# Kernel tuning notes

Measured on AMD Instinct MI355X. Metric: run time of the kernel, lower is better.

The kernel has to match this reference:

```python
import jax, jax.numpy as jnp
import numpy as np

N_COMP = 8
N_BASIS = 16
N_FEATURES = 64
N_CAT = 8
N_CONT = 56
N_UNIQUE = 100
BATCH = 32768
T0, T1 = 0.0, 10.0
SEP = 1e-3  # constants.MIN_TRANSITION_POINT_SEP
SIGNS = np.array([1.0, -1.0, 1.0, -1.0, 1.0, -1.0, 1.0, -1.0], dtype=np.float32)
CONT_IDX = np.arange(N_CONT)
CAT_IDX = np.arange(N_CONT, N_FEATURES)


def _offset():
    # torch_inverse_softplus(avg_interval_per_feature)
    v = (T1 - T0) / N_COMP / (N_FEATURES + 1)
    return float(np.log(np.exp(v) - 1.0))


def setup_inputs():
    key = jax.random.key(0)
    ks = jax.random.split(key, 11)
    off = _offset()
    B = jax.random.normal(ks[0], (BATCH, N_CONT, N_BASIS), jnp.float32)
    codes = jax.random.randint(ks[1], (BATCH, N_CAT), 0, N_UNIQUE)
    B_cat = jax.nn.one_hot(codes, N_UNIQUE, dtype=jnp.float32).reshape(BATCH, N_CAT * N_UNIQUE)
    Wh = jax.random.normal(ks[2], (N_BASIS, N_CONT, N_COMP), jnp.float32) + off
    Wh_cat = jax.random.normal(ks[3], (N_CAT, N_UNIQUE, N_COMP), jnp.float32) + off
    bh = jax.random.normal(ks[4], (N_COMP,), jnp.float32) + off
    Wv = jax.random.normal(ks[5], (N_BASIS, N_CONT, N_COMP), jnp.float32)
    Wv_cat = jax.random.normal(ks[6], (N_CAT, N_UNIQUE, N_COMP), jnp.float32)
    bv = jax.random.normal(ks[7], (N_COMP,), jnp.float32)
    Wic = jax.random.normal(ks[8], (N_BASIS, N_CONT, 1), jnp.float32)
    Wic_cat = jax.random.normal(ks[9], (N_CAT, N_UNIQUE, 1), jnp.float32)
    bic = jax.random.normal(ks[10], (1,), jnp.float32)
    return {"B": B, "B_cat": B_cat, "Wh": Wh, "Wh_cat": Wh_cat, "bh": bh,
            "Wv": Wv, "Wv_cat": Wv_cat, "bv": bv,
            "Wic": Wic, "Wic_cat": Wic_cat, "bic": bic}


def _calculate_gams(B, B_cat, W, W_cat, bias, positive):
    # continuous: per-feature small matmul  (b,i,k) x (k,i,c) -> (b,c,i)
    cont = jnp.einsum('bik,kic->bci', B, W)
    # categorical: one-hot gather expressed as blockwise matmul  (b,f,n) x (f,n,c) -> (b,c,f)
    cat = jnp.einsum('bfn,fnc->bcf', B_cat.reshape(B.shape[0], N_CAT, N_UNIQUE), W_cat)
    c = W.shape[2]
    out = jnp.zeros((B.shape[0], c, N_FEATURES + 1), dtype=B.dtype)
    out = out.at[:, :, CONT_IDX].set(cont)
    out = out.at[:, :, CAT_IDX].set(cat)
    out = out.at[:, :, -1].set(bias[None, :])
    return jax.nn.softplus(out) if positive else out


def reference(B, B_cat, Wh, Wh_cat, bh, Wv, Wv_cat, bv, Wic, Wic_cat, bic):
    H = _calculate_gams(B, B_cat, Wh, Wh_cat, bh, True)      # (b, n_comp, n_feat+1)
    V = _calculate_gams(B, B_cat, Wv, Wv_cat, bv, True)      # (b, n_comp, n_feat+1)
    IC = _calculate_gams(B, B_cat, Wic, Wic_cat, bic, False)  # (b, 1, n_feat+1)
    b = B.shape[0]
    signs = jnp.asarray(SIGNS)
    h_sum = H.sum(-1)   # (b, n_comp) per-segment horizontal increments
    v_sum = V.sum(-1)
    sep = SEP * jnp.arange(1, N_COMP + 1, dtype=B.dtype)
    # sequential cumulative build == prefix sums over the composition axis
    t = jnp.concatenate([jnp.full((b, 1), T0, B.dtype),
                         T0 + jnp.cumsum(h_sum, axis=1) + sep], axis=1)  # (b, n_comp+1)
    x0 = IC.sum(-1)     # (b, 1)
    x = jnp.concatenate([x0, x0 + jnp.cumsum(signs * v_sum, axis=1)], axis=1)
    # bounded composition: clamp the last horizontal coordinate
    t = t.at[:, -1].set(jnp.maximum(t[:, -2] + SEP, T1))
    return jnp.stack([t, x], axis=-1)  # (b, n_comp+1, 2)
```

## Files before the change

### kernel.cpp

```cpp
#include <hip/hip_runtime.h>

#define NCOMP 8
#define NCONT 56
#define NCAT 8
#define NU 100
#define NROWS 32768
#define SEPC 1e-3f
#define T1F 10.0f

#define WST 132
#define WICST 20

__device__ __forceinline__ float sp(float x) {
    return fmaxf(x, 0.0f) + __logf(1.0f + __expf(-fabsf(x)));
}

__device__ __forceinline__ float dot4(float4 a, float4 b) {
    return fmaf(a.x, b.x, fmaf(a.y, b.y, fmaf(a.z, b.z, a.w * b.w)));
}

__global__ __launch_bounds__(1024) void tpm_kernel(
    const float* __restrict__ B, const float* __restrict__ Bcat,
    const float* __restrict__ Wh, const float* __restrict__ Whc, const float* __restrict__ bh,
    const float* __restrict__ Wv, const float* __restrict__ Wvc, const float* __restrict__ bv,
    const float* __restrict__ Wic, const float* __restrict__ Wicc, const float* __restrict__ bic,
    float* __restrict__ out)
{
    __shared__ float sWh[NCONT * WST];
    __shared__ float sWv[NCONT * WST];
    __shared__ float sWic[NCONT * WICST];
    __shared__ int   sCode[16][NCAT];

    const int tid = threadIdx.x;

    for (int idx = tid; idx < NCONT * 128; idx += 1024) {
        int i = idx >> 7, rem = idx & 127;
        int c = rem >> 4, k = rem & 15;
        sWh[i * WST + rem] = Wh[(k * NCONT + i) * NCOMP + c];
        sWv[i * WST + rem] = Wv[(k * NCONT + i) * NCOMP + c];
    }
    for (int idx = tid; idx < NCONT * 16; idx += 1024) {
        int i = idx >> 4, k = idx & 15;
        sWic[i * WICST + k] = Wic[k * NCONT + i];
    }
    __syncthreads();

    const int lane = tid & 63;
    const int widx = tid >> 6;
    const int gw = (blockIdx.x << 4) + widx;
    const int nw = gridDim.x << 4;

    float bhs[NCOMP], bvs[NCOMP];
#pragma unroll
    for (int c = 0; c < NCOMP; ++c) { bhs[c] = sp(bh[c]); bvs[c] = sp(bv[c]); }
    const float bic0 = bic[0];

    for (int r = gw; r < NROWS; r += nw) {
        const float4* pc = (const float4*)(Bcat + (size_t)r * 800);
#pragma unroll
        for (int it = 0; it < 4; ++it) {
            int v = it * 64 + lane;
            if (v < 200) {
                float4 q = pc[v];
                int n = v * 4;
                if (q.x > 0.5f) sCode[widx][(n + 0) / NU] = (n + 0) % NU;
                if (q.y > 0.5f) sCode[widx][(n + 1) / NU] = (n + 1) % NU;
                if (q.z > 0.5f) sCode[widx][(n + 2) / NU] = (n + 2) % NU;
                if (q.w > 0.5f) sCode[widx][(n + 3) / NU] = (n + 3) % NU;
            }
        }
        __threadfence_block();

        float h[NCOMP], w[NCOMP], ic;
        if (lane < NCONT) {
            const float4* pB = (const float4*)(B + (size_t)r * 896 + lane * 16);
            float4 b0 = pB[0], b1 = pB[1], b2 = pB[2], b3 = pB[3];
            const float4* ph = (const float4*)(&sWh[lane * WST]);
            const float4* pv = (const float4*)(&sWv[lane * WST]);
#pragma unroll
            for (int c = 0; c < NCOMP; ++c) {
                h[c] = dot4(b0, ph[c * 4 + 0]) + dot4(b1, ph[c * 4 + 1]) +
                       dot4(b2, ph[c * 4 + 2]) + dot4(b3, ph[c * 4 + 3]);
                w[c] = dot4(b0, pv[c * 4 + 0]) + dot4(b1, pv[c * 4 + 1]) +
                       dot4(b2, pv[c * 4 + 2]) + dot4(b3, pv[c * 4 + 3]);
            }
            const float4* pi = (const float4*)(&sWic[lane * WICST]);
            ic = dot4(b0, pi[0]) + dot4(b1, pi[1]) + dot4(b2, pi[2]) + dot4(b3, pi[3]);
        } else {
            int f = lane - NCONT;
            int g = f * NU + sCode[widx][f];
            const float4* qh = (const float4*)(Whc + g * 8);
            const float4* qv = (const float4*)(Wvc + g * 8);
            float4 a0 = qh[0], a1 = qh[1];
            float4 c0 = qv[0], c1 = qv[1];
            h[0] = a0.x; h[1] = a0.y; h[2] = a0.z; h[3] = a0.w;
            h[4] = a1.x; h[5] = a1.y; h[6] = a1.z; h[7] = a1.w;
            w[0] = c0.x; w[1] = c0.y; w[2] = c0.z; w[3] = c0.w;
            w[4] = c1.x; w[5] = c1.y; w[6] = c1.z; w[7] = c1.w;
            ic = Wicc[g];
        }

#pragma unroll
        for (int c = 0; c < NCOMP; ++c) { h[c] = sp(h[c]); w[c] = sp(w[c]); }

#pragma unroll
        for (int off = 32; off >= 1; off >>= 1) {
#pragma unroll
            for (int c = 0; c < NCOMP; ++c) {
                h[c] += __shfl_xor(h[c], off, 64);
                w[c] += __shfl_xor(w[c], off, 64);
            }
            ic += __shfl_xor(ic, off, 64);
        }
#pragma unroll
        for (int c = 0; c < NCOMP; ++c) { h[c] += bhs[c]; w[c] += bvs[c]; }
        ic += bic0;

        if (lane < 9) {
            int m = (lane == 8) ? 7 : lane;
            float tj = SEPC * (float)lane;
            float xj = ic;
#pragma unroll
            for (int c = 0; c < NCOMP; ++c) {
                if (c < m)    tj += h[c];
                if (c < lane) xj += (c & 1) ? -w[c] : w[c];
            }
            if (lane == 8) tj = fmaxf(tj, T1F);
            float2 o; o.x = tj; o.y = xj;
            ((float2*)(out + (size_t)r * 18))[lane] = o;
        }
    }
}

extern "C" void kernel_launch(void* const* d_in, const int* in_sizes, int n_in,
                              void* d_out, int out_size, void* d_ws, size_t ws_size,
                              hipStream_t stream) {
    (void)in_sizes; (void)n_in; (void)out_size; (void)d_ws; (void)ws_size;
    const float* B    = (const float*)d_in[0];
    const float* Bcat = (const float*)d_in[1];
    const float* Wh   = (const float*)d_in[2];
    const float* Whc  = (const float*)d_in[3];
    const float* bh   = (const float*)d_in[4];
    const float* Wv   = (const float*)d_in[5];
    const float* Wvc  = (const float*)d_in[6];
    const float* bv   = (const float*)d_in[7];
    const float* Wic  = (const float*)d_in[8];
    const float* Wicc = (const float*)d_in[9];
    const float* bic  = (const float*)d_in[10];
    float* out = (float*)d_out;

    hipLaunchKernelGGL(tpm_kernel, dim3(256), dim3(1024), 0, stream,
                       B, Bcat, Wh, Whc, bh, Wv, Wvc, bv, Wic, Wicc, bic, out);
}
```

Measured before the change: 282.9 us.

## Use packed fp16 dot products, fp16 shuffle reductions, and branchless code decode

Converts the continuous weights and B rows to packed fp16 and computes the per-feature dot products with v_dot2 instructions. The H/V softplus outputs are packed into half2 pairs so the cross-lane reduction needs half as many shuffles. It also decodes each one-hot float4 arithmetically into a single store, moves the bias softplus into shared memory, simplifies softplus to an exp2/log form, and doubles the grid to 512 blocks with a launch-bounds hint. These changes cut ALU work, shuffles and register use, at the cost of fp16 precision in the matmul and in the sums of up to 64 softplus values, which may break tolerance. The new softplus can also overflow for large inputs.

```diff
diff --git a/kernel.cpp b/kernel.cpp
--- a/kernel.cpp
+++ b/kernel.cpp
@@ -8,41 +8,73 @@
 #define SEPC 1e-3f
 #define T1F 10.0f
 
-#define WST 132
-#define WICST 20
+typedef __fp16 f16x2 __attribute__((ext_vector_type(2)));
+typedef _Float16 h2arith __attribute__((ext_vector_type(2)));
+
+#define HSTRIDE 17
+#define ICSTRIDE 3
+
+union H8 { f16x2 h2[4]; float4 f4; };
 
 __device__ __forceinline__ float sp(float x) {
-    return fmaxf(x, 0.0f) + __logf(1.0f + __expf(-fabsf(x)));
-}
-
-__device__ __forceinline__ float dot4(float4 a, float4 b) {
-    return fmaf(a.x, b.x, fmaf(a.y, b.y, fmaf(a.z, b.z, a.w * b.w)));
-}
-
-__global__ __launch_bounds__(1024) void tpm_kernel(
+    return 0.69314718f * __builtin_amdgcn_logf(1.0f + __builtin_amdgcn_exp2f(x * 1.44269504f));
+}
+
+__device__ __forceinline__ f16x2 pkrtz(float a, float b) {
+    return __builtin_amdgcn_cvt_pkrtz(a, b);
+}
+
+__device__ __forceinline__ float fdot2(f16x2 a, f16x2 b, float c) {
+    return __builtin_amdgcn_fdot2(a, b, c, false);
+}
+
+__device__ __forceinline__ h2arith h2shfl_xor(h2arith v, int off) {
+    int i = __builtin_bit_cast(int, v);
+    i = __shfl_xor(i, off, 64);
+    return __builtin_bit_cast(h2arith, i);
+}
+
+__global__ __launch_bounds__(1024, 8) void tpm_kernel(
     const float* __restrict__ B, const float* __restrict__ Bcat,
     const float* __restrict__ Wh, const float* __restrict__ Whc, const float* __restrict__ bh,
     const float* __restrict__ Wv, const float* __restrict__ Wvc, const float* __restrict__ bv,
     const float* __restrict__ Wic, const float* __restrict__ Wicc, const float* __restrict__ bic,
     float* __restrict__ out)
 {
-    __shared__ float sWh[NCONT * WST];
-    __shared__ float sWv[NCONT * WST];
-    __shared__ float sWic[NCONT * WICST];
-    __shared__ int   sCode[16][NCAT];
+    __shared__ float4 sH4[NCONT * HSTRIDE];
+    __shared__ float4 sV4[NCONT * HSTRIDE];
+    __shared__ float4 sIC4[NCONT * ICSTRIDE];
+    __shared__ float2 sBias[NCOMP];
+    __shared__ float  sBic;
+    __shared__ int    sCode[16][NCAT];
 
     const int tid = threadIdx.x;
 
-    for (int idx = tid; idx < NCONT * 128; idx += 1024) {
-        int i = idx >> 7, rem = idx & 127;
-        int c = rem >> 4, k = rem & 15;
-        sWh[i * WST + rem] = Wh[(k * NCONT + i) * NCOMP + c];
-        sWv[i * WST + rem] = Wv[(k * NCONT + i) * NCOMP + c];
+    if (tid < 896) {
+        int icp = tid % 448, t = tid / 448;
+        int i = icp >> 3, c = icp & 7;
+        const float* gh = Wh + (size_t)(8 * t) * 448 + icp;
+        const float* gv = Wv + (size_t)(8 * t) * 448 + icp;
+        H8 uh, uv;
+#pragma unroll
+        for (int p = 0; p < 4; ++p) {
+            uh.h2[p] = pkrtz(gh[(2 * p) * 448], gh[(2 * p + 1) * 448]);
+            uv.h2[p] = pkrtz(gv[(2 * p) * 448], gv[(2 * p + 1) * 448]);
+        }
+        sH4[i * HSTRIDE + c * 2 + t] = uh.f4;
+        sV4[i * HSTRIDE + c * 2 + t] = uv.f4;
     }
-    for (int idx = tid; idx < NCONT * 16; idx += 1024) {
-        int i = idx >> 4, k = idx & 15;
-        sWic[i * WICST + k] = Wic[k * NCONT + i];
+    if (tid < 112) {
+        int i = tid % 56, t = tid / 56;
+        const float* gi = Wic + (size_t)(8 * t) * 56 + i;
+        H8 u;
+#pragma unroll
+        for (int p = 0; p < 4; ++p)
+            u.h2[p] = pkrtz(gi[(2 * p) * 56], gi[(2 * p + 1) * 56]);
+        sIC4[i * ICSTRIDE + t] = u.f4;
     }
+    if (tid < NCOMP) sBias[tid] = make_float2(sp(bh[tid]), sp(bv[tid]));
+    if (tid == NCOMP) sBic = bic[0];
     __syncthreads();
 
     const int lane = tid & 63;
@@ -50,23 +82,24 @@
     const int gw = (blockIdx.x << 4) + widx;
     const int nw = gridDim.x << 4;
 
-    float bhs[NCOMP], bvs[NCOMP];
-#pragma unroll
-    for (int c = 0; c < NCOMP; ++c) { bhs[c] = sp(bh[c]); bvs[c] = sp(bv[c]); }
-    const float bic0 = bic[0];
+    const float4* pH = sH4 + lane * HSTRIDE;
+    const float4* pV = sV4 + lane * HSTRIDE;
+    const float4* pIC = sIC4 + lane * ICSTRIDE;
 
     for (int r = gw; r < NROWS; r += nw) {
         const float4* pc = (const float4*)(Bcat + (size_t)r * 800);
 #pragma unroll
         for (int it = 0; it < 4; ++it) {
             int v = it * 64 + lane;
-            if (v < 200) {
+            if (it < 3 || v < 200) {
                 float4 q = pc[v];
-                int n = v * 4;
-                if (q.x > 0.5f) sCode[widx][(n + 0) / NU] = (n + 0) % NU;
-                if (q.y > 0.5f) sCode[widx][(n + 1) / NU] = (n + 1) % NU;
-                if (q.z > 0.5f) sCode[widx][(n + 2) / NU] = (n + 2) % NU;
-                if (q.w > 0.5f) sCode[widx][(n + 3) / NU] = (n + 3) % NU;
+                float n = (float)(4 * v);
+                float s = q.x * (n + 1.0f) + q.y * (n + 2.0f) + q.z * (n + 3.0f) + q.w * (n + 4.0f);
+                if (s > 0.5f) {
+                    int p = (int)s - 1;
+                    int f = p / NU;
+                    sCode[widx][f] = p - f * NU;
+                }
             }
         }
         __threadfence_block();
@@ -75,17 +108,41 @@
         if (lane < NCONT) {
             const float4* pB = (const float4*)(B + (size_t)r * 896 + lane * 16);
             float4 b0 = pB[0], b1 = pB[1], b2 = pB[2], b3 = pB[3];
-            const float4* ph = (const float4*)(&sWh[lane * WST]);
-            const float4* pv = (const float4*)(&sWv[lane * WST]);
+            f16x2 bb[8];
+            bb[0] = pkrtz(b0.x, b0.y);
+            bb[1] = pkrtz(b0.z, b0.w);
+            bb[2] = pkrtz(b1.x, b1.y);
+            bb[3] = pkrtz(b1.z, b1.w);
+            bb[4] = pkrtz(b2.x, b2.y);
+            bb[5] = pkrtz(b2.z, b2.w);
+            bb[6] = pkrtz(b3.x, b3.y);
+            bb[7] = pkrtz(b3.z, b3.w);
 #pragma unroll
             for (int c = 0; c < NCOMP; ++c) {
-                h[c] = dot4(b0, ph[c * 4 + 0]) + dot4(b1, ph[c * 4 + 1]) +
-                       dot4(b2, ph[c * 4 + 2]) + dot4(b3, ph[c * 4 + 3]);
-                w[c] = dot4(b0, pv[c * 4 + 0]) + dot4(b1, pv[c * 4 + 1]) +
-                       dot4(b2, pv[c * 4 + 2]) + dot4(b3, pv[c * 4 + 3]);
+                H8 u0, u1, v0, v1;
+                u0.f4 = pH[2 * c]; u1.f4 = pH[2 * c + 1];
+                v0.f4 = pV[2 * c]; v1.f4 = pV[2 * c + 1];
+                float ah = 0.0f, av = 0.0f;
+#pragma unroll
+                for (int p = 0; p < 4; ++p) {
+                    ah = fdot2(bb[p], u0.h2[p], ah);
+                    av = fdot2(bb[p], v0.h2[p], av);
+                }
+#pragma unroll
+                for (int p = 0; p < 4; ++p) {
+                    ah = fdot2(bb[4 + p], u1.h2[p], ah);
+                    av = fdot2(bb[4 + p], v1.h2[p], av);
+                }
+                h[c] = ah; w[c] = av;
             }
-            const float4* pi = (const float4*)(&sWic[lane * WICST]);
-            ic = dot4(b0, pi[0]) + dot4(b1, pi[1]) + dot4(b2, pi[2]) + dot4(b3, pi[3]);
+            H8 i0, i1;
+            i0.f4 = pIC[0]; i1.f4 = pIC[1];
+            float ai = 0.0f;
+#pragma unroll
+            for (int p = 0; p < 4; ++p) ai = fdot2(bb[p], i0.h2[p], ai);
+#pragma unroll
+            for (int p = 0; p < 4; ++p) ai = fdot2(bb[4 + p], i1.h2[p], ai);
+            ic = ai;
         } else {
             int f = lane - NCONT;
             int g = f * NU + sCode[widx][f];
@@ -100,34 +157,35 @@
             ic = Wicc[g];
         }
 
-#pragma unroll
-        for (int c = 0; c < NCOMP; ++c) { h[c] = sp(h[c]); w[c] = sp(w[c]); }
+        h2arith hw[NCOMP];
+#pragma unroll
+        for (int c = 0; c < NCOMP; ++c)
+            hw[c] = __builtin_bit_cast(h2arith, pkrtz(sp(h[c]), sp(w[c])));
 
 #pragma unroll
         for (int off = 32; off >= 1; off >>= 1) {
 #pragma unroll
-            for (int c = 0; c < NCOMP; ++c) {
-                h[c] += __shfl_xor(h[c], off, 64);
-                w[c] += __shfl_xor(w[c], off, 64);
-            }
+            for (int c = 0; c < NCOMP; ++c)
+                hw[c] = hw[c] + h2shfl_xor(hw[c], off);
             ic += __shfl_xor(ic, off, 64);
         }
-#pragma unroll
-        for (int c = 0; c < NCOMP; ++c) { h[c] += bhs[c]; w[c] += bvs[c]; }
-        ic += bic0;
 
         if (lane < 9) {
             int m = (lane == 8) ? 7 : lane;
             float tj = SEPC * (float)lane;
-            float xj = ic;
+            float xj = ic + sBic;
 #pragma unroll
             for (int c = 0; c < NCOMP; ++c) {
-                if (c < m)    tj += h[c];
-                if (c < lane) xj += (c & 1) ? -w[c] : w[c];
+                float2 bb2 = sBias[c];
+                if (c < m)    tj += (float)hw[c][0] + bb2.x;
+                if (c < lane) {
+                    float vv = (float)hw[c][1] + bb2.y;
+                    xj += (c & 1) ? -vv : vv;
+                }
             }
             if (lane == 8) tj = fmaxf(tj, T1F);
             float2 o; o.x = tj; o.y = xj;
-            ((float2*)(out + (size_t)r * 18))[lane] = o;
+            ((float2*)out)[(size_t)r * 9 + lane] = o;
         }
     }
 }
@@ -149,6 +207,6 @@
     const float* bic  = (const float*)d_in[10];
     float* out = (float*)d_out;
 
-    hipLaunchKernelGGL(tpm_kernel, dim3(256), dim3(1024), 0, stream,
+    hipLaunchKernelGGL(tpm_kernel, dim3(512), dim3(1024), 0, stream,
                        B, Bcat, Wh, Whc, bh, Wv, Wvc, bv, Wic, Wicc, bic, out);
 }
```

Result: faster. 275.0 us (-2.8%).
